# Kernel optimization log

Hardware: AMD Instinct MI355X
Metric: run time of the kernel (lower is better)

The kernel has to match this reference:

```python
import jax, jax.numpy as jnp
import numpy as np

N = 100000
E = 1600000
IN_DIM = 128
HID = 64
HEADS = 1
NEG_SLOPE = 0.2


def setup_inputs() -> dict:
    key = jax.random.key(0)
    ks = jax.random.split(key, 12)
    x = jax.random.normal(ks[0], (N, IN_DIM), dtype=jnp.float32)
    edge_index = jax.random.randint(ks[1], (2, E), 0, N, dtype=jnp.int64)
    s1 = 1.0 / np.sqrt(IN_DIM)
    s2 = 1.0 / np.sqrt(HEADS * HID)
    return {
        "x": x,
        "edge_index": edge_index,
        # layer 1: in_dim -> heads*hid
        "W1": jax.random.normal(ks[2], (IN_DIM, HEADS * HID), dtype=jnp.float32) * s1,
        "a_src1": jax.random.normal(ks[3], (HEADS, HID), dtype=jnp.float32) * s1,
        "a_dst1": jax.random.normal(ks[4], (HEADS, HID), dtype=jnp.float32) * s1,
        "b1": jnp.zeros((HEADS * HID,), dtype=jnp.float32),
        # layer 2: heads*hid -> hid (1 head)
        "W2": jax.random.normal(ks[5], (HEADS * HID, HID), dtype=jnp.float32) * s2,
        "a_src2": jax.random.normal(ks[6], (1, HID), dtype=jnp.float32) * s2,
        "a_dst2": jax.random.normal(ks[7], (1, HID), dtype=jnp.float32) * s2,
        "b2": jnp.zeros((HID,), dtype=jnp.float32),
        # output head
        "W_out": jax.random.normal(ks[8], (HID, 1), dtype=jnp.float32) * (1.0 / np.sqrt(HID)),
        "b_out": jnp.zeros((1,), dtype=jnp.float32),
    }


def _gat_conv(x, src, dst, W, a_src, a_dst, bias, heads, hid):
    n = x.shape[0]
    h = (x @ W).reshape(n, heads, hid)                      # [N, H, D]
    alpha_s = jnp.einsum("nhd,hd->nh", h, a_src)            # [N, H]
    alpha_d = jnp.einsum("nhd,hd->nh", h, a_dst)
    e = alpha_s[src] + alpha_d[dst]                          # [E, H]
    e = jax.nn.leaky_relu(e, NEG_SLOPE)
    # segment softmax over edges sharing the same destination node
    m = jax.ops.segment_max(e, dst, num_segments=n)          # [N, H]
    ex = jnp.exp(e - m[dst])
    denom = jax.ops.segment_sum(ex, dst, num_segments=n)     # [N, H]
    alpha = ex / denom[dst]                                  # [E, H]
    out = jax.ops.segment_sum(h[src] * alpha[:, :, None], dst, num_segments=n)
    return out.reshape(n, heads * hid) + bias


def reference(x, edge_index, W1, a_src1, a_dst1, b1, W2, a_src2, a_dst2, b2, W_out, b_out):
    n = x.shape[0]
    # PyG GATConv default add_self_loops=True
    loops = jnp.arange(n, dtype=edge_index.dtype)
    src = jnp.concatenate([edge_index[0], loops])
    dst = jnp.concatenate([edge_index[1], loops])
    h = jax.nn.elu(_gat_conv(x, src, dst, W1, a_src1, a_dst1, b1, HEADS, HID))
    h = jax.nn.elu(_gat_conv(h, src, dst, W2, a_src2, a_dst2, b2, 1, HID))
    return (h @ W_out + b_out).squeeze(-1)                   # [N]
```

## Files before the change

kernel.cpp:

```cpp
#include <hip/hip_runtime.h>
#include <hip/hip_fp16.h>
#include <math.h>

#define NEG_SLOPE 0.2f
#define BKT_SHIFT 8
#define BKT_NODES (1 << BKT_SHIFT)
#define BKT_CAP 512
#define BKT_FCAP 6144
#define P1_CHUNK 4096

typedef _Float16 f16x8 __attribute__((ext_vector_type(8)));
typedef float    f32x4 __attribute__((ext_vector_type(4)));
union FU  { uint4 u; f16x8 f; };
union H2U { __half2 h; unsigned u; };

__device__ __forceinline__ float lrelu(float x){ return fmaxf(x, NEG_SLOPE * x); }
__device__ __forceinline__ float elu_fast(float x){
  float t = __expf(fminf(x, 0.f)) - 1.f;
  return x > 0.f ? x : t;
}


__global__ __launch_bounds__(256) void k_p1(const int* __restrict__ src, const int* __restrict__ dst,
                                            int E, int B, int* __restrict__ bktCur,
                                            unsigned* __restrict__ pairs,
                                            const float* __restrict__ W1, const float* __restrict__ W2,
                                            uint4* __restrict__ W1f, uint4* __restrict__ W2f){
  __shared__ int h[BKT_CAP], base[BKT_CAP], cur[BKT_CAP];
  int tid = threadIdx.x;
  if (blockIdx.x == 0){
    for (int idx = tid; idx < 16 * 64; idx += 256){
      int lane = idx & 63, fs = idx >> 6;
      int t = fs >> 2, s = fs & 3;
      int m = lane & 15, quad = lane >> 4;
      f16x8 v;
      #pragma unroll
      for (int j = 0; j < 8; ++j)
        v[j] = (_Float16)W1[(s * 32 + quad * 8 + j) * 64 + t * 16 + m];
      FU fu; fu.f = v;
      W1f[fs * 64 + lane] = fu.u;
    }
    for (int idx = tid; idx < 8 * 64; idx += 256){
      int lane = idx & 63, fs = idx >> 6;
      int t = fs >> 1, s = fs & 1;
      int m = lane & 15, quad = lane >> 4;
      f16x8 v;
      #pragma unroll
      for (int j = 0; j < 8; ++j)
        v[j] = (_Float16)W2[(s * 32 + quad * 8 + j) * 64 + t * 16 + m];
      FU fu; fu.f = v;
      W2f[fs * 64 + lane] = fu.u;
    }
  }
  for (int i = tid; i < BKT_CAP; i += 256){ h[i] = 0; cur[i] = 0; }
  __syncthreads();
  int beg = blockIdx.x * P1_CHUNK;
  int end = min(beg + P1_CHUNK, E);
  int m4 = (end - beg) >> 2;
  const int4* d4 = (const int4*)(dst + beg);
  const int4* s4 = (const int4*)(src + beg);
  for (int i = tid; i < m4; i += 256){
    int4 d = d4[i];
    atomicAdd(&h[d.x >> BKT_SHIFT], 1); atomicAdd(&h[d.y >> BKT_SHIFT], 1);
    atomicAdd(&h[d.z >> BKT_SHIFT], 1); atomicAdd(&h[d.w >> BKT_SHIFT], 1);
  }
  for (int i = beg + (m4 << 2) + tid; i < end; i += 256)
    atomicAdd(&h[dst[i] >> BKT_SHIFT], 1);
  __syncthreads();
  for (int i = tid; i < B; i += 256)
    if (h[i]) base[i] = i * BKT_FCAP + atomicAdd(&bktCur[i], h[i]);
  __syncthreads();
  for (int i = tid; i < m4; i += 256){
    int4 d = d4[i]; int4 s = s4[i];
    int b0 = d.x >> BKT_SHIFT, b1 = d.y >> BKT_SHIFT, b2 = d.z >> BKT_SHIFT, b3 = d.w >> BKT_SHIFT;
    int p0 = base[b0] + atomicAdd(&cur[b0], 1);
    pairs[p0] = ((unsigned)(d.x & (BKT_NODES-1)) << 17) | (unsigned)s.x;
    int p1 = base[b1] + atomicAdd(&cur[b1], 1);
    pairs[p1] = ((unsigned)(d.y & (BKT_NODES-1)) << 17) | (unsigned)s.y;
    int p2 = base[b2] + atomicAdd(&cur[b2], 1);
    pairs[p2] = ((unsigned)(d.z & (BKT_NODES-1)) << 17) | (unsigned)s.z;
    int p3 = base[b3] + atomicAdd(&cur[b3], 1);
    pairs[p3] = ((unsigned)(d.w & (BKT_NODES-1)) << 17) | (unsigned)s.w;
  }
  for (int i = beg + (m4 << 2) + tid; i < end; i += 256){
    int d = dst[i], s = src[i];
    int b = d >> BKT_SHIFT;
    int p = base[b] + atomicAdd(&cur[b], 1);
    pairs[p] = ((unsigned)(d & (BKT_NODES-1)) << 17) | (unsigned)s;
  }
}

__global__ __launch_bounds__(256) void k_p2(const unsigned* __restrict__ pairs,
                                            const int* __restrict__ bktCur,
                                            int N, int2* __restrict__ offs2, int* __restrict__ col){
  __shared__ int sc[BKT_NODES], cu[BKT_NODES];
  int b = blockIdx.x, tid = threadIdx.x;
  int nbase = b << BKT_SHIFT;
  int bs = b * BKT_FCAP;
  int be = bs + bktCur[b];
  sc[tid] = 0;
  __syncthreads();
  for (int i = bs + tid; i < be; i += 256)
    atomicAdd(&sc[pairs[i] >> 17], 1);
  __syncthreads();
  int v = sc[tid];
  for (int o = 1; o < 256; o <<= 1){
    int x = (tid >= o) ? sc[tid - o] : 0;
    __syncthreads();
    sc[tid] += x;
    __syncthreads();
  }
  int ex = sc[tid] - v;
  cu[tid] = bs + ex;
  if (nbase + tid < N) offs2[nbase + tid] = make_int2(bs + ex, bs + ex + v);
  __syncthreads();
  for (int i = bs + tid; i < be; i += 256){
    unsigned pr = pairs[i];
    int p = atomicAdd(&cu[pr >> 17], 1);
    col[p] = (int)(pr & 0x1FFFFu);
  }
}

__global__ __launch_bounds__(256) void k_mgemm1(
    const float* __restrict__ X, const uint4* __restrict__ Wf,
    const float* __restrict__ a_src, const float* __restrict__ a_dst,
    uint2* __restrict__ H, float* __restrict__ as_, float* __restrict__ ad_, int n)
{
  int lane = threadIdx.x & 63, wv = threadIdx.x >> 6;
  int quad = lane >> 4, nn = lane & 15;
  int rowb = blockIdx.x * 64 + wv * 16;
  int row = rowb + nn;
  bool ok = row < n;
  int rowc = ok ? row : n - 1;

  f16x8 af[4][4];
  #pragma unroll
  for (int t = 0; t < 4; ++t)
    #pragma unroll
    for (int s = 0; s < 4; ++s){
      FU fu; fu.u = Wf[(t * 4 + s) * 64 + lane];
      af[t][s] = fu.f;
    }

  const float4* Xr = (const float4*)(X + (size_t)rowc * 128);
  float4 xb[4][2];
  #pragma unroll
  for (int s = 0; s < 4; ++s){
    xb[s][0] = Xr[s * 8 + quad * 2];
    xb[s][1] = Xr[s * 8 + quad * 2 + 1];
  }

  f32x4 acc[4] = {};
  #pragma unroll
  for (int s = 0; s < 4; ++s){
    f16x8 bf;
    bf[0] = (_Float16)xb[s][0].x; bf[1] = (_Float16)xb[s][0].y;
    bf[2] = (_Float16)xb[s][0].z; bf[3] = (_Float16)xb[s][0].w;
    bf[4] = (_Float16)xb[s][1].x; bf[5] = (_Float16)xb[s][1].y;
    bf[6] = (_Float16)xb[s][1].z; bf[7] = (_Float16)xb[s][1].w;
    #pragma unroll
    for (int t = 0; t < 4; ++t)
      acc[t] = __builtin_amdgcn_mfma_f32_16x16x32_f16(af[t][s], bf, acc[t], 0, 0, 0);
  }

  if (ok){
    #pragma unroll
    for (int t = 0; t < 4; ++t){
      H2U p0, p1;
      p0.h = __floats2half2_rn(acc[t][0], acc[t][1]);
      p1.h = __floats2half2_rn(acc[t][2], acc[t][3]);
      H[(size_t)row * 16 + t * 4 + quad] = make_uint2(p0.u, p1.u);
    }
  }
  float sl = 0.f, dl = 0.f;
  #pragma unroll
  for (int t = 0; t < 4; ++t){
    float4 a4 = ((const float4*)a_src)[t * 4 + quad];
    float4 d4 = ((const float4*)a_dst)[t * 4 + quad];
    sl += acc[t][0] * a4.x + acc[t][1] * a4.y + acc[t][2] * a4.z + acc[t][3] * a4.w;
    dl += acc[t][0] * d4.x + acc[t][1] * d4.y + acc[t][2] * d4.z + acc[t][3] * d4.w;
  }
  sl += __shfl_xor(sl, 16, 64); sl += __shfl_xor(sl, 32, 64);
  dl += __shfl_xor(dl, 16, 64); dl += __shfl_xor(dl, 32, 64);
  if (lane < 16 && ok){ as_[row] = sl; ad_[row] = dl; }
}

__global__ __launch_bounds__(256) void k_mgemm2(
    const uint4* __restrict__ Xh, const uint4* __restrict__ Wf,
    const float* __restrict__ a_src, const float* __restrict__ a_dst,
    uint2* __restrict__ H, float* __restrict__ as_, float* __restrict__ ad_, int n)
{
  int lane = threadIdx.x & 63, wv = threadIdx.x >> 6;
  int quad = lane >> 4, nn = lane & 15;
  int rowb = blockIdx.x * 64 + wv * 16;
  int row = rowb + nn;
  bool ok = row < n;
  int rowc = ok ? row : n - 1;

  f16x8 af[4][2];
  #pragma unroll
  for (int t = 0; t < 4; ++t)
    #pragma unroll
    for (int s = 0; s < 2; ++s){
      FU fu; fu.u = Wf[(t * 2 + s) * 64 + lane];
      af[t][s] = fu.f;
    }

  f16x8 bf[2];
  #pragma unroll
  for (int s = 0; s < 2; ++s){
    FU fu; fu.u = Xh[(size_t)rowc * 8 + s * 4 + quad];
    bf[s] = fu.f;
  }

  f32x4 acc[4] = {};
  #pragma unroll
  for (int s = 0; s < 2; ++s)
    #pragma unroll
    for (int t = 0; t < 4; ++t)
      acc[t] = __builtin_amdgcn_mfma_f32_16x16x32_f16(af[t][s], bf[s], acc[t], 0, 0, 0);

  if (ok){
    #pragma unroll
    for (int t = 0; t < 4; ++t){
      H2U p0, p1;
      p0.h = __floats2half2_rn(acc[t][0], acc[t][1]);
      p1.h = __floats2half2_rn(acc[t][2], acc[t][3]);
      H[(size_t)row * 16 + t * 4 + quad] = make_uint2(p0.u, p1.u);
    }
  }
  float sl = 0.f, dl = 0.f;
  #pragma unroll
  for (int t = 0; t < 4; ++t){
    float4 a4 = ((const float4*)a_src)[t * 4 + quad];
    float4 d4 = ((const float4*)a_dst)[t * 4 + quad];
    sl += acc[t][0] * a4.x + acc[t][1] * a4.y + acc[t][2] * a4.z + acc[t][3] * a4.w;
    dl += acc[t][0] * d4.x + acc[t][1] * d4.y + acc[t][2] * d4.z + acc[t][3] * d4.w;
  }
  sl += __shfl_xor(sl, 16, 64); sl += __shfl_xor(sl, 32, 64);
  dl += __shfl_xor(dl, 16, 64); dl += __shfl_xor(dl, 32, 64);
  if (lane < 16 && ok){ as_[row] = sl; ad_[row] = dl; }
}

#define FMA8(e, hv) { const __half2* hp = (const __half2*)&(hv);               \
  a[0]=fmaf(e, __half2float(hp[0].x), a[0]); a[1]=fmaf(e, __half2float(hp[0].y), a[1]); \
  a[2]=fmaf(e, __half2float(hp[1].x), a[2]); a[3]=fmaf(e, __half2float(hp[1].y), a[3]); \
  a[4]=fmaf(e, __half2float(hp[2].x), a[4]); a[5]=fmaf(e, __half2float(hp[2].y), a[5]); \
  a[6]=fmaf(e, __half2float(hp[3].x), a[6]); a[7]=fmaf(e, __half2float(hp[3].y), a[7]); }

#define AGG_BODY \
  int lane = threadIdx.x & 63, w = threadIdx.x >> 6;                           \
  int m = lane >> 3, c8 = lane & 7;                                            \
  int node0 = blockIdx.x * 32 + w * 8 + m;                                     \
  bool ok = node0 < n;                                                         \
  int node = ok ? node0 : n - 1;                                               \
  int2 be2 = offs2[node];                                                      \
  int beg = be2.x, d = be2.y - be2.x;                                          \
  int maxd = d;                                                                \
  maxd = max(maxd, __shfl_xor(maxd, 8, 64));                                   \
  maxd = max(maxd, __shfl_xor(maxd, 16, 64));                                  \
  maxd = max(maxd, __shfl_xor(maxd, 32, 64));                                  \
  float adv = ad_[node];                                                       \
  float exs = __expf(lrelu(as_[node] + adv));                                  \
  uint4 hself = H4[(size_t)node * 8 + c8];                                     \
  float denom = exs;                                                           \
  float a[8];                                                                  \
  { const __half2* hp = (const __half2*)&hself;                                \
    _Pragma("unroll")                                                          \
    for (int i = 0; i < 4; ++i){                                               \
      a[2*i]   = exs * __half2float(hp[i].x);                                  \
      a[2*i+1] = exs * __half2float(hp[i].y);                                  \
    } }                                                                        \
  for (int j = 0; j < maxd; j += 4){                                           \
    int ss[4]; float asv[4]; uint4 hv[4];                                      \
    _Pragma("unroll")                                                          \
    for (int u = 0; u < 4; ++u) ss[u] = (j + u < d) ? col[beg + j + u] : 0;    \
    _Pragma("unroll")                                                          \
    for (int u = 0; u < 4; ++u) asv[u] = as_[ss[u]];                           \
    _Pragma("unroll")                                                          \
    for (int u = 0; u < 4; ++u) hv[u] = H4[(size_t)ss[u] * 8 + c8];            \
    _Pragma("unroll")                                                          \
    for (int u = 0; u < 4; ++u){                                               \
      float e = (j + u < d) ? __expf(lrelu(asv[u] + adv)) : 0.f;               \
      denom += e;                                                              \
      FMA8(e, hv[u])                                                           \
    }                                                                          \
  }

__global__ __launch_bounds__(256) void k_agg1(
    const int2* __restrict__ offs2, const int* __restrict__ col,
    const uint4* __restrict__ H4, const float* __restrict__ as_, const float* __restrict__ ad_,
    const float* __restrict__ bias, uint4* __restrict__ outH, int n)
{
  AGG_BODY
  float inv = 1.f / denom;
  float4 b0 = *(const float4*)&bias[8 * c8];
  float4 b1 = *(const float4*)&bias[8 * c8 + 4];
  float bb[8] = {b0.x, b0.y, b0.z, b0.w, b1.x, b1.y, b1.z, b1.w};
  unsigned oh[4];
  #pragma unroll
  for (int i = 0; i < 4; ++i){
    float v0 = elu_fast(fmaf(a[2*i],   inv, bb[2*i]));
    float v1 = elu_fast(fmaf(a[2*i+1], inv, bb[2*i+1]));
    __half2 h = __floats2half2_rn(v0, v1);
    oh[i] = *(unsigned*)&h;
  }
  if (ok){
    uint4 ov; ov.x = oh[0]; ov.y = oh[1]; ov.z = oh[2]; ov.w = oh[3];
    outH[(size_t)node * 8 + c8] = ov;
  }
}

__global__ __launch_bounds__(256) void k_agg2(
    const int2* __restrict__ offs2, const int* __restrict__ col,
    const uint4* __restrict__ H4, const float* __restrict__ as_, const float* __restrict__ ad_,
    const float* __restrict__ bias, const float* __restrict__ Wout, const float* __restrict__ bout,
    float* __restrict__ out, int n)
{
  AGG_BODY
  float inv = 1.f / denom;
  float4 b0 = *(const float4*)&bias[8 * c8];
  float4 b1 = *(const float4*)&bias[8 * c8 + 4];
  float4 w0 = *(const float4*)&Wout[8 * c8];
  float4 w1 = *(const float4*)&Wout[8 * c8 + 4];
  float bb[8] = {b0.x, b0.y, b0.z, b0.w, b1.x, b1.y, b1.z, b1.w};
  float ww[8] = {w0.x, w0.y, w0.z, w0.w, w1.x, w1.y, w1.z, w1.w};
  float p = 0.f;
  #pragma unroll
  for (int i = 0; i < 8; ++i)
    p += elu_fast(fmaf(a[i], inv, bb[i])) * ww[i];
  p += __shfl_xor(p, 1, 64); p += __shfl_xor(p, 2, 64); p += __shfl_xor(p, 4, 64);
  if (c8 == 0 && ok) out[node] = p + bout[0];
}

extern "C" void kernel_launch(void* const* d_in, const int* in_sizes, int n_in,
                              void* d_out, int out_size, void* d_ws, size_t ws_size,
                              hipStream_t stream)
{
  const float* x    = (const float*)d_in[0];
  const int*   ei   = (const int*)d_in[1];
  const float* W1   = (const float*)d_in[2];
  const float* as1w = (const float*)d_in[3];
  const float* ad1w = (const float*)d_in[4];
  const float* b1   = (const float*)d_in[5];
  const float* W2   = (const float*)d_in[6];
  const float* as2w = (const float*)d_in[7];
  const float* ad2w = (const float*)d_in[8];
  const float* b2   = (const float*)d_in[9];
  const float* Wout = (const float*)d_in[10];
  const float* bout = (const float*)d_in[11];
  float* out = (float*)d_out;

  const int N = in_sizes[0] / 128;
  const int E = in_sizes[1] / 2;
  const int* srcA = ei;
  const int* dstA = ei + E;
  const int B = (N + BKT_NODES - 1) >> BKT_SHIFT;

  char* p = (char*)d_ws;
  auto alloc = [&](size_t bytes){ char* r = p; p += (bytes + 255) & ~255ull; return r; };
  int*   bktCur = (int*)alloc(BKT_CAP * 4);
  int2*  offs2  = (int2*)alloc((size_t)N * 8);
  int*   col    = (int*)alloc((size_t)B * BKT_FCAP * 4);
  float* vas1 = (float*)alloc((size_t)N * 4);
  float* vad1 = (float*)alloc((size_t)N * 4);
  float* vas2 = (float*)alloc((size_t)N * 4);
  float* vad2 = (float*)alloc((size_t)N * 4);
  uint4* w1f  = (uint4*)alloc(16 * 64 * 16);
  uint4* w2f  = (uint4*)alloc(8 * 64 * 16);
  uint2* h1   = (uint2*)alloc((size_t)N * 64 * 2);
  uint2* h1e  = (uint2*)alloc((size_t)N * 64 * 2);
  unsigned* pairs = (unsigned*)h1;
  uint2* h2   = h1;

  hipMemsetAsync(bktCur, 0, BKT_CAP * 4, stream);

  int nchunk = (E + P1_CHUNK - 1) / P1_CHUNK;
  k_p1<<<nchunk, 256, 0, stream>>>(srcA, dstA, E, B, bktCur, pairs, W1, W2, w1f, w2f);
  k_p2<<<B, 256, 0, stream>>>(pairs, bktCur, N, offs2, col);

  int gblocks = (N + 63) / 64;
  k_mgemm1<<<gblocks, 256, 0, stream>>>(x, w1f, as1w, ad1w, h1, vas1, vad1, N);
  k_agg1  <<<(N + 31) / 32, 256, 0, stream>>>(offs2, col, (const uint4*)h1, vas1, vad1, b1, (uint4*)h1e, N);
  k_mgemm2<<<gblocks, 256, 0, stream>>>((const uint4*)h1e, w2f, as2w, ad2w, h2, vas2, vad2, N);
  k_agg2  <<<(N + 31) / 32, 256, 0, stream>>>(offs2, col, (const uint4*)h2, vas2, vad2, b2, Wout, bout, out, N);
}
```

Baseline: 244.2 us.

## Sort nodes by degree per bucket, fuse CSR build with GEMM1, widen gather unroll

Within each 256-node bucket, the CSR build pass now also computes a degree-binned permutation. The aggregation kernels use it to process nodes with similar degree together in one wavefront, which reduces lane divergence from uneven neighbor counts. When workspace allows, the pairs buffer gets its own allocation so the CSR build and the first GEMM can run as one fused launch instead of two serialized kernels. The gather loop unroll goes from 4 to 8 to put more loads in flight. The cost is extra per-node indirection through perm, scattered output writes, and higher register pressure.

```diff
diff --git a/kernel.cpp b/kernel.cpp
--- a/kernel.cpp
+++ b/kernel.cpp
@@ -90,15 +90,18 @@
   }
 }
 
-__global__ __launch_bounds__(256) void k_p2(const unsigned* __restrict__ pairs,
-                                            const int* __restrict__ bktCur,
-                                            int N, int2* __restrict__ offs2, int* __restrict__ col){
+__device__ __forceinline__ void p2_body(const unsigned* __restrict__ pairs,
+                                        const int* __restrict__ bktCur,
+                                        int N, int2* __restrict__ offs2,
+                                        int* __restrict__ col, int* __restrict__ perm, int b){
   __shared__ int sc[BKT_NODES], cu[BKT_NODES];
-  int b = blockIdx.x, tid = threadIdx.x;
+  __shared__ int dbase[65], dcur[65];
+  int tid = threadIdx.x;
   int nbase = b << BKT_SHIFT;
   int bs = b * BKT_FCAP;
   int be = bs + bktCur[b];
   sc[tid] = 0;
+  if (tid < 65) dcur[tid] = 0;
   __syncthreads();
   for (int i = bs + tid; i < be; i += 256)
     atomicAdd(&sc[pairs[i] >> 17], 1);
@@ -112,8 +115,27 @@
   }
   int ex = sc[tid] - v;
   cu[tid] = bs + ex;
-  if (nbase + tid < N) offs2[nbase + tid] = make_int2(bs + ex, bs + ex + v);
-  __syncthreads();
+  bool valid = (nbase + tid) < N;
+  if (valid) offs2[nbase + tid] = make_int2(bs + ex, bs + ex + v);
+  int bin = valid ? min(v, 63) : 64;
+  atomicAdd(&dcur[bin], 1);
+  __syncthreads();
+  if (tid < 64){
+    int x = dcur[tid];
+    int s = x;
+    for (int o = 1; o < 64; o <<= 1){
+      int y = __shfl_up(s, (unsigned)o, 64);
+      if (tid >= o) s += y;
+    }
+    dbase[tid] = s - x;
+  }
+  __syncthreads();
+  if (tid < 65) dcur[tid] = 0;
+  __syncthreads();
+  if (valid){
+    int r = dbase[bin] + atomicAdd(&dcur[bin], 1);
+    perm[nbase + r] = nbase + tid;
+  }
   for (int i = bs + tid; i < be; i += 256){
     unsigned pr = pairs[i];
     int p = atomicAdd(&cu[pr >> 17], 1);
@@ -121,8 +143,100 @@
   }
 }
 
+__global__ __launch_bounds__(256) void k_p2(const unsigned* __restrict__ pairs,
+                                            const int* __restrict__ bktCur,
+                                            int N, int2* __restrict__ offs2,
+                                            int* __restrict__ col, int* __restrict__ perm){
+  p2_body(pairs, bktCur, N, offs2, col, perm, blockIdx.x);
+}
+
+__device__ __forceinline__ void mg1_body(
+    const float* __restrict__ X, const uint4* __restrict__ Wf,
+    const float* __restrict__ a_src, const float* __restrict__ a_dst,
+    uint2* __restrict__ H, float* __restrict__ as_, float* __restrict__ ad_, int n, int bb)
+{
+  int lane = threadIdx.x & 63, wv = threadIdx.x >> 6;
+  int quad = lane >> 4, nn = lane & 15;
+  int rowb = bb * 64 + wv * 16;
+  int row = rowb + nn;
+  bool ok = row < n;
+  int rowc = ok ? row : n - 1;
+
+  f16x8 af[4][4];
+  #pragma unroll
+  for (int t = 0; t < 4; ++t)
+    #pragma unroll
+    for (int s = 0; s < 4; ++s){
+      FU fu; fu.u = Wf[(t * 4 + s) * 64 + lane];
+      af[t][s] = fu.f;
+    }
+
+  const float4* Xr = (const float4*)(X + (size_t)rowc * 128);
+  float4 xb[4][2];
+  #pragma unroll
+  for (int s = 0; s < 4; ++s){
+    xb[s][0] = Xr[s * 8 + quad * 2];
+    xb[s][1] = Xr[s * 8 + quad * 2 + 1];
+  }
+
+  f32x4 acc[4] = {};
+  #pragma unroll
+  for (int s = 0; s < 4; ++s){
+    f16x8 bf;
+    bf[0] = (_Float16)xb[s][0].x; bf[1] = (_Float16)xb[s][0].y;
+    bf[2] = (_Float16)xb[s][0].z; bf[3] = (_Float16)xb[s][0].w;
+    bf[4] = (_Float16)xb[s][1].x; bf[5] = (_Float16)xb[s][1].y;
+    bf[6] = (_Float16)xb[s][1].z; bf[7] = (_Float16)xb[s][1].w;
+    #pragma unroll
+    for (int t = 0; t < 4; ++t)
+      acc[t] = __builtin_amdgcn_mfma_f32_16x16x32_f16(af[t][s], bf, acc[t], 0, 0, 0);
+  }
+
+  if (ok){
+    #pragma unroll
+    for (int t = 0; t < 4; ++t){
+      H2U p0, p1;
+      p0.h = __floats2half2_rn(acc[t][0], acc[t][1]);
+      p1.h = __floats2half2_rn(acc[t][2], acc[t][3]);
+      H[(size_t)row * 16 + t * 4 + quad] = make_uint2(p0.u, p1.u);
+    }
+  }
+  float sl = 0.f, dl = 0.f;
+  #pragma unroll
+  for (int t = 0; t < 4; ++t){
+    float4 a4 = ((const float4*)a_src)[t * 4 + quad];
+    float4 d4 = ((const float4*)a_dst)[t * 4 + quad];
+    sl += acc[t][0] * a4.x + acc[t][1] * a4.y + acc[t][2] * a4.z + acc[t][3] * a4.w;
+    dl += acc[t][0] * d4.x + acc[t][1] * d4.y + acc[t][2] * d4.z + acc[t][3] * d4.w;
+  }
+  sl += __shfl_xor(sl, 16, 64); sl += __shfl_xor(sl, 32, 64);
+  dl += __shfl_xor(dl, 16, 64); dl += __shfl_xor(dl, 32, 64);
+  if (lane < 16 && ok){ as_[row] = sl; ad_[row] = dl; }
+}
+
 __global__ __launch_bounds__(256) void k_mgemm1(
     const float* __restrict__ X, const uint4* __restrict__ Wf,
+    const float* __restrict__ a_src, const float* __restrict__ a_dst,
+    uint2* __restrict__ H, float* __restrict__ as_, float* __restrict__ ad_, int n)
+{
+  mg1_body(X, Wf, a_src, a_dst, H, as_, ad_, n, blockIdx.x);
+}
+
+__global__ __launch_bounds__(256) void k_fused(
+    const unsigned* __restrict__ pairs, const int* __restrict__ bktCur,
+    int N, int2* __restrict__ offs2, int* __restrict__ col, int* __restrict__ perm, int p2B,
+    const float* __restrict__ X, const uint4* __restrict__ Wf,
+    const float* __restrict__ a_src, const float* __restrict__ a_dst,
+    uint2* __restrict__ H, float* __restrict__ as_, float* __restrict__ ad_)
+{
+  if ((int)blockIdx.x < p2B)
+    p2_body(pairs, bktCur, N, offs2, col, perm, blockIdx.x);
+  else
+    mg1_body(X, Wf, a_src, a_dst, H, as_, ad_, N, blockIdx.x - p2B);
+}
+
+__global__ __launch_bounds__(256) void k_mgemm2(
+    const uint4* __restrict__ Xh, const uint4* __restrict__ Wf,
     const float* __restrict__ a_src, const float* __restrict__ a_dst,
     uint2* __restrict__ H, float* __restrict__ as_, float* __restrict__ ad_, int n)
 {
@@ -133,35 +247,28 @@
   bool ok = row < n;
   int rowc = ok ? row : n - 1;
 
-  f16x8 af[4][4];
+  f16x8 af[4][2];
   #pragma unroll
   for (int t = 0; t < 4; ++t)
     #pragma unroll
-    for (int s = 0; s < 4; ++s){
-      FU fu; fu.u = Wf[(t * 4 + s) * 64 + lane];
+    for (int s = 0; s < 2; ++s){
+      FU fu; fu.u = Wf[(t * 2 + s) * 64 + lane];
       af[t][s] = fu.f;
     }
 
-  const float4* Xr = (const float4*)(X + (size_t)rowc * 128);
-  float4 xb[4][2];
-  #pragma unroll
-  for (int s = 0; s < 4; ++s){
-    xb[s][0] = Xr[s * 8 + quad * 2];
-    xb[s][1] = Xr[s * 8 + quad * 2 + 1];
+  f16x8 bf[2];
+  #pragma unroll
+  for (int s = 0; s < 2; ++s){
+    FU fu; fu.u = Xh[(size_t)rowc * 8 + s * 4 + quad];
+    bf[s] = fu.f;
   }
 
   f32x4 acc[4] = {};
   #pragma unroll
-  for (int s = 0; s < 4; ++s){
-    f16x8 bf;
-    bf[0] = (_Float16)xb[s][0].x; bf[1] = (_Float16)xb[s][0].y;
-    bf[2] = (_Float16)xb[s][0].z; bf[3] = (_Float16)xb[s][0].w;
-    bf[4] = (_Float16)xb[s][1].x; bf[5] = (_Float16)xb[s][1].y;
-    bf[6] = (_Float16)xb[s][1].z; bf[7] = (_Float16)xb[s][1].w;
+  for (int s = 0; s < 2; ++s)
     #pragma unroll
     for (int t = 0; t < 4; ++t)
-      acc[t] = __builtin_amdgcn_mfma_f32_16x16x32_f16(af[t][s], bf, acc[t], 0, 0, 0);
-  }
+      acc[t] = __builtin_amdgcn_mfma_f32_16x16x32_f16(af[t][s], bf[s], acc[t], 0, 0, 0);
 
   if (ok){
     #pragma unroll
@@ -185,63 +292,6 @@
   if (lane < 16 && ok){ as_[row] = sl; ad_[row] = dl; }
 }
 
-__global__ __launch_bounds__(256) void k_mgemm2(
-    const uint4* __restrict__ Xh, const uint4* __restrict__ Wf,
-    const float* __restrict__ a_src, const float* __restrict__ a_dst,
-    uint2* __restrict__ H, float* __restrict__ as_, float* __restrict__ ad_, int n)
-{
-  int lane = threadIdx.x & 63, wv = threadIdx.x >> 6;
-  int quad = lane >> 4, nn = lane & 15;
-  int rowb = blockIdx.x * 64 + wv * 16;
-  int row = rowb + nn;
-  bool ok = row < n;
-  int rowc = ok ? row : n - 1;
-
-  f16x8 af[4][2];
-  #pragma unroll
-  for (int t = 0; t < 4; ++t)
-    #pragma unroll
-    for (int s = 0; s < 2; ++s){
-      FU fu; fu.u = Wf[(t * 2 + s) * 64 + lane];
-      af[t][s] = fu.f;
-    }
-
-  f16x8 bf[2];
-  #pragma unroll
-  for (int s = 0; s < 2; ++s){
-    FU fu; fu.u = Xh[(size_t)rowc * 8 + s * 4 + quad];
-    bf[s] = fu.f;
-  }
-
-  f32x4 acc[4] = {};
-  #pragma unroll
-  for (int s = 0; s < 2; ++s)
-    #pragma unroll
-    for (int t = 0; t < 4; ++t)
-      acc[t] = __builtin_amdgcn_mfma_f32_16x16x32_f16(af[t][s], bf[s], acc[t], 0, 0, 0);
-
-  if (ok){
-    #pragma unroll
-    for (int t = 0; t < 4; ++t){
-      H2U p0, p1;
-      p0.h = __floats2half2_rn(acc[t][0], acc[t][1]);
-      p1.h = __floats2half2_rn(acc[t][2], acc[t][3]);
-      H[(size_t)row * 16 + t * 4 + quad] = make_uint2(p0.u, p1.u);
-    }
-  }
-  float sl = 0.f, dl = 0.f;
-  #pragma unroll
-  for (int t = 0; t < 4; ++t){
-    float4 a4 = ((const float4*)a_src)[t * 4 + quad];
-    float4 d4 = ((const float4*)a_dst)[t * 4 + quad];
-    sl += acc[t][0] * a4.x + acc[t][1] * a4.y + acc[t][2] * a4.z + acc[t][3] * a4.w;
-    dl += acc[t][0] * d4.x + acc[t][1] * d4.y + acc[t][2] * d4.z + acc[t][3] * d4.w;
-  }
-  sl += __shfl_xor(sl, 16, 64); sl += __shfl_xor(sl, 32, 64);
-  dl += __shfl_xor(dl, 16, 64); dl += __shfl_xor(dl, 32, 64);
-  if (lane < 16 && ok){ as_[row] = sl; ad_[row] = dl; }
-}
-
 #define FMA8(e, hv) { const __half2* hp = (const __half2*)&(hv);               \
   a[0]=fmaf(e, __half2float(hp[0].x), a[0]); a[1]=fmaf(e, __half2float(hp[0].y), a[1]); \
   a[2]=fmaf(e, __half2float(hp[1].x), a[2]); a[3]=fmaf(e, __half2float(hp[1].y), a[3]); \
@@ -253,7 +303,7 @@
   int m = lane >> 3, c8 = lane & 7;                                            \
   int node0 = blockIdx.x * 32 + w * 8 + m;                                     \
   bool ok = node0 < n;                                                         \
-  int node = ok ? node0 : n - 1;                                               \
+  int node = perm[ok ? node0 : 0];                                             \
   int2 be2 = offs2[node];                                                      \
   int beg = be2.x, d = be2.y - be2.x;                                          \
   int maxd = d;                                                                \
@@ -271,16 +321,16 @@
       a[2*i]   = exs * __half2float(hp[i].x);                                  \
       a[2*i+1] = exs * __half2float(hp[i].y);                                  \
     } }                                                                        \
-  for (int j = 0; j < maxd; j += 4){                                           \
-    int ss[4]; float asv[4]; uint4 hv[4];                                      \
+  for (int j = 0; j < maxd; j += 8){                                           \
+    int ss[8]; float asv[8]; uint4 hv[8];                                      \
     _Pragma("unroll")                                                          \
-    for (int u = 0; u < 4; ++u) ss[u] = (j + u < d) ? col[beg + j + u] : 0;    \
+    for (int u = 0; u < 8; ++u) ss[u] = (j + u < d) ? col[beg + j + u] : 0;    \
     _Pragma("unroll")                                                          \
-    for (int u = 0; u < 4; ++u) asv[u] = as_[ss[u]];                           \
+    for (int u = 0; u < 8; ++u) asv[u] = as_[ss[u]];                           \
     _Pragma("unroll")                                                          \
-    for (int u = 0; u < 4; ++u) hv[u] = H4[(size_t)ss[u] * 8 + c8];            \
+    for (int u = 0; u < 8; ++u) hv[u] = H4[(size_t)ss[u] * 8 + c8];            \
     _Pragma("unroll")                                                          \
-    for (int u = 0; u < 4; ++u){                                               \
+    for (int u = 0; u < 8; ++u){                                               \
       float e = (j + u < d) ? __expf(lrelu(asv[u] + adv)) : 0.f;               \
       denom += e;                                                              \
       FMA8(e, hv[u])                                                           \
@@ -288,7 +338,7 @@
   }
 
 __global__ __launch_bounds__(256) void k_agg1(
-    const int2* __restrict__ offs2, const int* __restrict__ col,
+    const int2* __restrict__ offs2, const int* __restrict__ col, const int* __restrict__ perm,
     const uint4* __restrict__ H4, const float* __restrict__ as_, const float* __restrict__ ad_,
     const float* __restrict__ bias, uint4* __restrict__ outH, int n)
 {
@@ -312,7 +362,7 @@
 }
 
 __global__ __launch_bounds__(256) void k_agg2(
-    const int2* __restrict__ offs2, const int* __restrict__ col,
+    const int2* __restrict__ offs2, const int* __restrict__ col, const int* __restrict__ perm,
     const uint4* __restrict__ H4, const float* __restrict__ as_, const float* __restrict__ ad_,
     const float* __restrict__ bias, const float* __restrict__ Wout, const float* __restrict__ bout,
     float* __restrict__ out, int n)
@@ -357,7 +407,8 @@
   const int* dstA = ei + E;
   const int B = (N + BKT_NODES - 1) >> BKT_SHIFT;
 
-  char* p = (char*)d_ws;
+  char* p0 = (char*)d_ws;
+  char* p = p0;
   auto alloc = [&](size_t bytes){ char* r = p; p += (bytes + 255) & ~255ull; return r; };
   int*   bktCur = (int*)alloc(BKT_CAP * 4);
   int2*  offs2  = (int2*)alloc((size_t)N * 8);
@@ -370,18 +421,35 @@
   uint4* w2f  = (uint4*)alloc(8 * 64 * 16);
   uint2* h1   = (uint2*)alloc((size_t)N * 64 * 2);
   uint2* h1e  = (uint2*)alloc((size_t)N * 64 * 2);
-  unsigned* pairs = (unsigned*)h1;
+  int*   perm = (int*)alloc((size_t)N * 4);
   uint2* h2   = h1;
+
+  size_t pairsBytes = (size_t)B * BKT_FCAP * 4;
+  size_t used = (size_t)(p - p0);
+  unsigned* pairs;
+  bool fused;
+  if (used + pairsBytes + 256 <= ws_size){
+    pairs = (unsigned*)alloc(pairsBytes);
+    fused = true;
+  } else {
+    pairs = (unsigned*)h1;
+    fused = false;
+  }
 
   hipMemsetAsync(bktCur, 0, BKT_CAP * 4, stream);
 
   int nchunk = (E + P1_CHUNK - 1) / P1_CHUNK;
   k_p1<<<nchunk, 256, 0, stream>>>(srcA, dstA, E, B, bktCur, pairs, W1, W2, w1f, w2f);
-  k_p2<<<B, 256, 0, stream>>>(pairs, bktCur, N, offs2, col);
 
   int gblocks = (N + 63) / 64;
-  k_mgemm1<<<gblocks, 256, 0, stream>>>(x, w1f, as1w, ad1w, h1, vas1, vad1, N);
-  k_agg1  <<<(N + 31) / 32, 256, 0, stream>>>(offs2, col, (const uint4*)h1, vas1, vad1, b1, (uint4*)h1e, N);
+  if (fused){
+    k_fused<<<B + gblocks, 256, 0, stream>>>(pairs, bktCur, N, offs2, col, perm, B,
+                                             x, w1f, as1w, ad1w, h1, vas1, vad1);
+  } else {
+    k_p2<<<B, 256, 0, stream>>>(pairs, bktCur, N, offs2, col, perm);
+    k_mgemm1<<<gblocks, 256, 0, stream>>>(x, w1f, as1w, ad1w, h1, vas1, vad1, N);
+  }
+  k_agg1  <<<(N + 31) / 32, 256, 0, stream>>>(offs2, col, perm, (const uint4*)h1, vas1, vad1, b1, (uint4*)h1e, N);
   k_mgemm2<<<gblocks, 256, 0, stream>>>((const uint4*)h1e, w2f, as2w, ad2w, h2, vas2, vad2, N);
-  k_agg2  <<<(N + 31) / 32, 256, 0, stream>>>(offs2, col, (const uint4*)h2, vas2, vad2, b2, Wout, bout, out, N);
-}
+  k_agg2  <<<(N + 31) / 32, 256, 0, stream>>>(offs2, col, perm, (const uint4*)h2, vas2, vad2, b2, Wout, bout, out, N);
+}
```

Measured after the change: 266.0 us. +9.0%, slower.

## Shard bucket atomic counters four ways and aggregate two node groups per block

Applied to the files above, without the earlier changes.

Each destination bucket's global fill counter is split into four shards chosen by block index, with each shard owning a quarter of the bucket's capacity. This is meant to reduce contention on the global atomics during edge bucketing, and the CSR build pass now walks all four shards. The aggregation kernels also process two groups of 32 nodes per block, which halves the grid and reuses the bias/weight loads. The risk is overflow, since each shard holds only 1536 entries per bucket, and the serialized node groups leave less parallelism for hiding gather latency.

```diff
diff --git a/kernel.cpp b/kernel.cpp
--- a/kernel.cpp
+++ b/kernel.cpp
@@ -7,6 +7,7 @@
 #define BKT_NODES (1 << BKT_SHIFT)
 #define BKT_CAP 512
 #define BKT_FCAP 6144
+#define BKT_SHARD (BKT_FCAP / 4)
 #define P1_CHUNK 4096
 
 typedef _Float16 f16x8 __attribute__((ext_vector_type(8)));
@@ -56,6 +57,7 @@
   __syncthreads();
   int beg = blockIdx.x * P1_CHUNK;
   int end = min(beg + P1_CHUNK, E);
+  int shard = blockIdx.x & 3;
   int m4 = (end - beg) >> 2;
   const int4* d4 = (const int4*)(dst + beg);
   const int4* s4 = (const int4*)(src + beg);
@@ -68,7 +70,7 @@
     atomicAdd(&h[dst[i] >> BKT_SHIFT], 1);
   __syncthreads();
   for (int i = tid; i < B; i += 256)
-    if (h[i]) base[i] = i * BKT_FCAP + atomicAdd(&bktCur[i], h[i]);
+    if (h[i]) base[i] = i * BKT_FCAP + shard * BKT_SHARD + atomicAdd(&bktCur[i * 4 + shard], h[i]);
   __syncthreads();
   for (int i = tid; i < m4; i += 256){
     int4 d = d4[i]; int4 s = s4[i];
@@ -97,11 +99,15 @@
   int b = blockIdx.x, tid = threadIdx.x;
   int nbase = b << BKT_SHIFT;
   int bs = b * BKT_FCAP;
-  int be = bs + bktCur[b];
   sc[tid] = 0;
   __syncthreads();
-  for (int i = bs + tid; i < be; i += 256)
-    atomicAdd(&sc[pairs[i] >> 17], 1);
+  #pragma unroll
+  for (int s = 0; s < 4; ++s){
+    int ss_ = bs + s * BKT_SHARD;
+    int se_ = ss_ + bktCur[b * 4 + s];
+    for (int i = ss_ + tid; i < se_; i += 256)
+      atomicAdd(&sc[pairs[i] >> 17], 1);
+  }
   __syncthreads();
   int v = sc[tid];
   for (int o = 1; o < 256; o <<= 1){
@@ -114,10 +120,15 @@
   cu[tid] = bs + ex;
   if (nbase + tid < N) offs2[nbase + tid] = make_int2(bs + ex, bs + ex + v);
   __syncthreads();
-  for (int i = bs + tid; i < be; i += 256){
-    unsigned pr = pairs[i];
-    int p = atomicAdd(&cu[pr >> 17], 1);
-    col[p] = (int)(pr & 0x1FFFFu);
+  #pragma unroll
+  for (int s = 0; s < 4; ++s){
+    int ss_ = bs + s * BKT_SHARD;
+    int se_ = ss_ + bktCur[b * 4 + s];
+    for (int i = ss_ + tid; i < se_; i += 256){
+      unsigned pr = pairs[i];
+      int p = atomicAdd(&cu[pr >> 17], 1);
+      col[p] = (int)(pr & 0x1FFFFu);
+    }
   }
 }
 
@@ -248,66 +259,74 @@
   a[4]=fmaf(e, __half2float(hp[2].x), a[4]); a[5]=fmaf(e, __half2float(hp[2].y), a[5]); \
   a[6]=fmaf(e, __half2float(hp[3].x), a[6]); a[7]=fmaf(e, __half2float(hp[3].y), a[7]); }
 
-#define AGG_BODY \
-  int lane = threadIdx.x & 63, w = threadIdx.x >> 6;                           \
-  int m = lane >> 3, c8 = lane & 7;                                            \
-  int node0 = blockIdx.x * 32 + w * 8 + m;                                     \
-  bool ok = node0 < n;                                                         \
-  int node = ok ? node0 : n - 1;                                               \
-  int2 be2 = offs2[node];                                                      \
-  int beg = be2.x, d = be2.y - be2.x;                                          \
-  int maxd = d;                                                                \
-  maxd = max(maxd, __shfl_xor(maxd, 8, 64));                                   \
-  maxd = max(maxd, __shfl_xor(maxd, 16, 64));                                  \
-  maxd = max(maxd, __shfl_xor(maxd, 32, 64));                                  \
-  float adv = ad_[node];                                                       \
-  float exs = __expf(lrelu(as_[node] + adv));                                  \
-  uint4 hself = H4[(size_t)node * 8 + c8];                                     \
-  float denom = exs;                                                           \
-  float a[8];                                                                  \
-  { const __half2* hp = (const __half2*)&hself;                                \
-    _Pragma("unroll")                                                          \
-    for (int i = 0; i < 4; ++i){                                               \
-      a[2*i]   = exs * __half2float(hp[i].x);                                  \
-      a[2*i+1] = exs * __half2float(hp[i].y);                                  \
-    } }                                                                        \
-  for (int j = 0; j < maxd; j += 4){                                           \
-    int ss[4]; float asv[4]; uint4 hv[4];                                      \
-    _Pragma("unroll")                                                          \
-    for (int u = 0; u < 4; ++u) ss[u] = (j + u < d) ? col[beg + j + u] : 0;    \
-    _Pragma("unroll")                                                          \
-    for (int u = 0; u < 4; ++u) asv[u] = as_[ss[u]];                           \
-    _Pragma("unroll")                                                          \
-    for (int u = 0; u < 4; ++u) hv[u] = H4[(size_t)ss[u] * 8 + c8];            \
-    _Pragma("unroll")                                                          \
-    for (int u = 0; u < 4; ++u){                                               \
-      float e = (j + u < d) ? __expf(lrelu(asv[u] + adv)) : 0.f;               \
-      denom += e;                                                              \
-      FMA8(e, hv[u])                                                           \
-    }                                                                          \
-  }
+__device__ __forceinline__ void agg_core(
+    const int2* __restrict__ offs2, const int* __restrict__ col,
+    const uint4* __restrict__ H4, const float* __restrict__ as_, const float* __restrict__ ad_,
+    int node, int c8, float& denom, float a[8])
+{
+  int2 be2 = offs2[node];
+  int beg = be2.x, d = be2.y - be2.x;
+  int maxd = d;
+  maxd = max(maxd, __shfl_xor(maxd, 8, 64));
+  maxd = max(maxd, __shfl_xor(maxd, 16, 64));
+  maxd = max(maxd, __shfl_xor(maxd, 32, 64));
+  float adv = ad_[node];
+  float exs = __expf(lrelu(as_[node] + adv));
+  uint4 hself = H4[(size_t)node * 8 + c8];
+  denom = exs;
+  { const __half2* hp = (const __half2*)&hself;
+    #pragma unroll
+    for (int i = 0; i < 4; ++i){
+      a[2*i]   = exs * __half2float(hp[i].x);
+      a[2*i+1] = exs * __half2float(hp[i].y);
+    } }
+  for (int j = 0; j < maxd; j += 4){
+    int ss[4]; float asv[4]; uint4 hv[4];
+    #pragma unroll
+    for (int u = 0; u < 4; ++u) ss[u] = (j + u < d) ? col[beg + j + u] : 0;
+    #pragma unroll
+    for (int u = 0; u < 4; ++u) asv[u] = as_[ss[u]];
+    #pragma unroll
+    for (int u = 0; u < 4; ++u) hv[u] = H4[(size_t)ss[u] * 8 + c8];
+    #pragma unroll
+    for (int u = 0; u < 4; ++u){
+      float e = (j + u < d) ? __expf(lrelu(asv[u] + adv)) : 0.f;
+      denom += e;
+      FMA8(e, hv[u])
+    }
+  }
+}
 
 __global__ __launch_bounds__(256) void k_agg1(
     const int2* __restrict__ offs2, const int* __restrict__ col,
     const uint4* __restrict__ H4, const float* __restrict__ as_, const float* __restrict__ ad_,
     const float* __restrict__ bias, uint4* __restrict__ outH, int n)
 {
-  AGG_BODY
-  float inv = 1.f / denom;
+  int lane = threadIdx.x & 63, w = threadIdx.x >> 6;
+  int m = lane >> 3, c8 = lane & 7;
   float4 b0 = *(const float4*)&bias[8 * c8];
   float4 b1 = *(const float4*)&bias[8 * c8 + 4];
   float bb[8] = {b0.x, b0.y, b0.z, b0.w, b1.x, b1.y, b1.z, b1.w};
-  unsigned oh[4];
-  #pragma unroll
-  for (int i = 0; i < 4; ++i){
-    float v0 = elu_fast(fmaf(a[2*i],   inv, bb[2*i]));
-    float v1 = elu_fast(fmaf(a[2*i+1], inv, bb[2*i+1]));
-    __half2 h = __floats2half2_rn(v0, v1);
-    oh[i] = *(unsigned*)&h;
-  }
-  if (ok){
-    uint4 ov; ov.x = oh[0]; ov.y = oh[1]; ov.z = oh[2]; ov.w = oh[3];
-    outH[(size_t)node * 8 + c8] = ov;
+  #pragma unroll
+  for (int g = 0; g < 2; ++g){
+    int node0 = blockIdx.x * 64 + g * 32 + w * 8 + m;
+    bool ok = node0 < n;
+    int node = ok ? node0 : n - 1;
+    float denom; float a[8];
+    agg_core(offs2, col, H4, as_, ad_, node, c8, denom, a);
+    float inv = 1.f / denom;
+    unsigned oh[4];
+    #pragma unroll
+    for (int i = 0; i < 4; ++i){
+      float v0 = elu_fast(fmaf(a[2*i],   inv, bb[2*i]));
+      float v1 = elu_fast(fmaf(a[2*i+1], inv, bb[2*i+1]));
+      __half2 h = __floats2half2_rn(v0, v1);
+      oh[i] = *(unsigned*)&h;
+    }
+    if (ok){
+      uint4 ov; ov.x = oh[0]; ov.y = oh[1]; ov.z = oh[2]; ov.w = oh[3];
+      outH[(size_t)node * 8 + c8] = ov;
+    }
   }
 }
 
@@ -317,20 +336,29 @@
     const float* __restrict__ bias, const float* __restrict__ Wout, const float* __restrict__ bout,
     float* __restrict__ out, int n)
 {
-  AGG_BODY
-  float inv = 1.f / denom;
+  int lane = threadIdx.x & 63, w = threadIdx.x >> 6;
+  int m = lane >> 3, c8 = lane & 7;
   float4 b0 = *(const float4*)&bias[8 * c8];
   float4 b1 = *(const float4*)&bias[8 * c8 + 4];
   float4 w0 = *(const float4*)&Wout[8 * c8];
   float4 w1 = *(const float4*)&Wout[8 * c8 + 4];
   float bb[8] = {b0.x, b0.y, b0.z, b0.w, b1.x, b1.y, b1.z, b1.w};
   float ww[8] = {w0.x, w0.y, w0.z, w0.w, w1.x, w1.y, w1.z, w1.w};
-  float p = 0.f;
-  #pragma unroll
-  for (int i = 0; i < 8; ++i)
-    p += elu_fast(fmaf(a[i], inv, bb[i])) * ww[i];
-  p += __shfl_xor(p, 1, 64); p += __shfl_xor(p, 2, 64); p += __shfl_xor(p, 4, 64);
-  if (c8 == 0 && ok) out[node] = p + bout[0];
+  #pragma unroll
+  for (int g = 0; g < 2; ++g){
+    int node0 = blockIdx.x * 64 + g * 32 + w * 8 + m;
+    bool ok = node0 < n;
+    int node = ok ? node0 : n - 1;
+    float denom; float a[8];
+    agg_core(offs2, col, H4, as_, ad_, node, c8, denom, a);
+    float inv = 1.f / denom;
+    float p = 0.f;
+    #pragma unroll
+    for (int i = 0; i < 8; ++i)
+      p += elu_fast(fmaf(a[i], inv, bb[i])) * ww[i];
+    p += __shfl_xor(p, 1, 64); p += __shfl_xor(p, 2, 64); p += __shfl_xor(p, 4, 64);
+    if (c8 == 0 && ok) out[node] = p + bout[0];
+  }
 }
 
 extern "C" void kernel_launch(void* const* d_in, const int* in_sizes, int n_in,
@@ -359,7 +387,7 @@
 
   char* p = (char*)d_ws;
   auto alloc = [&](size_t bytes){ char* r = p; p += (bytes + 255) & ~255ull; return r; };
-  int*   bktCur = (int*)alloc(BKT_CAP * 4);
+  int*   bktCur = (int*)alloc(BKT_CAP * 4 * 4);
   int2*  offs2  = (int2*)alloc((size_t)N * 8);
   int*   col    = (int*)alloc((size_t)B * BKT_FCAP * 4);
   float* vas1 = (float*)alloc((size_t)N * 4);
@@ -373,15 +401,16 @@
   unsigned* pairs = (unsigned*)h1;
   uint2* h2   = h1;
 
-  hipMemsetAsync(bktCur, 0, BKT_CAP * 4, stream);
+  hipMemsetAsync(bktCur, 0, BKT_CAP * 4 * 4, stream);
 
   int nchunk = (E + P1_CHUNK - 1) / P1_CHUNK;
   k_p1<<<nchunk, 256, 0, stream>>>(srcA, dstA, E, B, bktCur, pairs, W1, W2, w1f, w2f);
   k_p2<<<B, 256, 0, stream>>>(pairs, bktCur, N, offs2, col);
 
   int gblocks = (N + 63) / 64;
+  int ablocks = (N + 63) / 64;
   k_mgemm1<<<gblocks, 256, 0, stream>>>(x, w1f, as1w, ad1w, h1, vas1, vad1, N);
-  k_agg1  <<<(N + 31) / 32, 256, 0, stream>>>(offs2, col, (const uint4*)h1, vas1, vad1, b1, (uint4*)h1e, N);
+  k_agg1  <<<ablocks, 256, 0, stream>>>(offs2, col, (const uint4*)h1, vas1, vad1, b1, (uint4*)h1e, N);
   k_mgemm2<<<gblocks, 256, 0, stream>>>((const uint4*)h1e, w2f, as2w, ad2w, h2, vas2, vad2, N);
-  k_agg2  <<<(N + 31) / 32, 256, 0, stream>>>(offs2, col, (const uint4*)h2, vas2, vad2, b2, Wout, bout, out, N);
-}
+  k_agg2  <<<ablocks, 256, 0, stream>>>(offs2, col, (const uint4*)h2, vas2, vad2, b2, Wout, bout, out, N);
+}
```

New measurement: 258.4 us. 5.8% more time.
